# Kernel tuning notes

Measured on AMD Instinct MI355X. Metric: run time of the kernel, lower is better.

Reference implementation:

```python
import math
import jax, jax.numpy as jnp
import numpy as np
from jax import lax

RAY_START, RAY_END = 0.5, 2.5
N_PLANES = 32

# ---- camera constants (faithful to pose_spherical / fibonacci_sphere / ImagePlanes init) ----

def _pose_spherical_np(theta, phi, radius):
    trans_t = np.array([[1,0,0,0],[0,1,0,0],[0,0,1,radius],[0,0,0,1]], dtype=np.float64)
    p = phi/180.0*np.pi
    rot_phi = np.array([[1,0,0,0],[0,np.cos(p),-np.sin(p),0],[0,np.sin(p),np.cos(p),0],[0,0,0,1]], dtype=np.float64)
    t = theta/180.0*np.pi
    rot_theta = np.array([[np.cos(t),0,-np.sin(t),0],[0,1,0,0],[np.sin(t),0,np.cos(t),0],[0,0,0,1]], dtype=np.float64)
    e = 90.0/180.0*np.pi
    rot_eta = np.array([[np.cos(e),np.sin(e),0,0],[-np.sin(e),np.cos(e),0,0],[0,0,1,0],[0,0,0,1]], dtype=np.float64)
    c2w = rot_eta @ (rot_theta @ (rot_phi @ trans_t))
    return np.array([[-1,0,0,0],[0,0,1,0],[0,1,0,0],[0,0,0,1]], dtype=np.float64) @ c2w

def _fibonacci_sphere(n):
    pts = []
    golden = math.pi*(math.sqrt(5.0)-1.0)
    for i in range(n):
        y = 1 - (i/float(n-1))*2
        r = math.sqrt(1-y*y)
        th = golden*i
        x, z = math.cos(th)*r, math.sin(th)*r
        pts.append((math.atan2(z, math.sqrt(x*x+y*y)), math.atan2(y, x)))
    return pts

_poses = np.stack([_pose_spherical_np(theta, phi, -1.307) for phi, theta in _fibonacci_sphere(N_PLANES)])
_flip = np.diag(np.array([-1.0,1.0,1.0,1.0]))
POSES34 = jnp.asarray(np.stack([np.linalg.inv(p @ _flip)[:3] for p in _poses]).astype(np.float32))  # [32,3,4]
KMAT = jnp.asarray(np.array([[1.0254,0,0.5],[0,1.0254,0.5],[0,0,1]], dtype=np.float32))  # [3,3]

# ---- grid_sample(bilinear, zeros, align_corners=False) ----

def _grid_sample(img, grid):
    # img [C,H,W], grid [P,2] (x,y) in [-1,1] -> [C,P]
    C, H, W = img.shape
    ix = ((grid[:, 0] + 1.0)*W - 1.0)*0.5
    iy = ((grid[:, 1] + 1.0)*H - 1.0)*0.5
    x0 = jnp.floor(ix); y0 = jnp.floor(iy)
    wx1 = ix - x0; wy1 = iy - y0
    def tap(xx, yy, w):
        valid = (xx >= 0) & (xx <= W - 1) & (yy >= 0) & (yy <= H - 1)
        xi = jnp.clip(xx, 0, W - 1).astype(jnp.int32)
        yi = jnp.clip(yy, 0, H - 1).astype(jnp.int32)
        return img[:, yi, xi] * (w*valid)[None, :]
    return (tap(x0, y0, (1-wx1)*(1-wy1)) + tap(x0+1, y0, wx1*(1-wy1))
            + tap(x0, y0+1, (1-wx1)*wy1) + tap(x0+1, y0+1, wx1*wy1))

# ---- ImagePlanes.forward ----

def _image_plane_feats(images, points):
    # images [32,3,H,W], points [P,3] -> [P, 96+64]
    P = points.shape[0]
    ph = jnp.concatenate([points, jnp.ones((P, 1), points.dtype)], axis=1)  # [P,4]
    cam = jnp.einsum('kij,pj->kip', POSES34, ph)            # [32,3,P]
    ps = jnp.einsum('ij,kjp->kip', KMAT, cam)                # [32,3,P]
    pix = jnp.clip(ps[:, :2, :] / ps[:, 2:3, :], 0.0, 1.0)*2.0 - 1.0  # [32,2,P]
    grid = jnp.transpose(pix, (0, 2, 1))                     # [32,P,2]
    feats = jax.vmap(_grid_sample)(images, grid)             # [32,3,P]
    feats = jnp.transpose(feats, (2, 0, 1)).reshape(P, -1)   # [P,96] plane-major
    pixflat = jnp.transpose(grid, (1, 0, 2)).reshape(P, -1)  # [P,64]
    return jnp.concatenate([feats, pixflat], axis=1)

# ---- RenderNetwork.forward (only self.net path is used) ----

def _decode(x, W1, b1, W2, b2):
    h = jax.nn.softplus(x @ W1 + b1)
    o = h @ W2 + b2
    rgb = jax.nn.sigmoid(o[..., 1:])*(1.0 + 2*0.001) - 0.001
    return rgb, o[..., 0:1]

# ---- MipRayMarcher2 ----

def _ray_march(colors, densities, depths):
    deltas = depths[:, :, 1:] - depths[:, :, :-1]
    cm = (colors[:, :, :-1] + colors[:, :, 1:])*0.5
    dm = (densities[:, :, :-1] + densities[:, :, 1:])*0.5
    zm = (depths[:, :, :-1] + depths[:, :, 1:])*0.5
    dm = jax.nn.softplus(dm - 1.0)
    alpha = 1.0 - jnp.exp(-dm*deltas)
    shifted = jnp.concatenate([jnp.ones_like(alpha[:, :, :1]), 1.0 - alpha + 1e-10], axis=2)
    weights = alpha * jnp.cumprod(shifted, axis=2)[:, :, :-1]
    rgb = jnp.sum(weights*cm, axis=2)*2.0 - 1.0
    wtot = jnp.sum(weights, axis=2)
    depth = jnp.sum(weights*zm, axis=2)/wtot
    depth = jnp.clip(jnp.where(jnp.isnan(depth), jnp.inf, depth), jnp.min(depths), jnp.max(depths))
    return rgb, depth, weights

# ---- importance sampling (sample_pdf + maxpool/avgpool smoothing) ----

def _sample_pdf(bins, weights, u, eps=1e-5):
    M = weights.shape[-1]
    weights = weights + eps
    pdf = weights / jnp.sum(weights, -1, keepdims=True)
    cdf = jnp.cumsum(pdf, -1)
    cdf = jnp.concatenate([jnp.zeros_like(cdf[:, :1]), cdf], -1)  # [R,M+1]
    inds = jax.vmap(lambda c, uu: jnp.searchsorted(c, uu, side='right'))(cdf, u)
    below = jnp.maximum(inds - 1, 0)
    above = jnp.minimum(inds, M)
    cdf_b = jnp.take_along_axis(cdf, below, 1)
    cdf_a = jnp.take_along_axis(cdf, above, 1)
    bins_b = jnp.take_along_axis(bins, below, 1)
    bins_a = jnp.take_along_axis(bins, above, 1)
    denom = jnp.where(cdf_a - cdf_b < eps, 1.0, cdf_a - cdf_b)
    return bins_b + (u - cdf_b)/denom*(bins_a - bins_b)

def _sample_importance(z_vals, weights, n_imp, u):
    B, N, S, _ = z_vals.shape
    z = z_vals.reshape(B*N, S)
    w = weights.reshape(B*N, S - 1)
    wp = jnp.pad(w, ((0, 0), (1, 1)), constant_values=-jnp.inf)
    m = jnp.maximum(wp[:, :-1], wp[:, 1:])          # max_pool1d(k=2,s=1,p=1)
    sm = (m[:, :-1] + m[:, 1:])*0.5 + 0.01           # avg_pool1d(k=2,s=1)
    samples = _sample_pdf(z, sm[:, 1:-1], u.reshape(B*N, n_imp))
    return lax.stop_gradient(samples).reshape(B, N, n_imp, 1)

# ---- full ImportanceRenderer.forward ----

def _forward(planes, ray_origins, ray_directions, strat_noise, pdf_u, W1, b1, W2, b2, D, n_imp):
    B, N = ray_origins.shape[0], ray_origins.shape[1]
    H, Wd = planes.shape[-2], planes.shape[-1]
    images = planes.reshape(B, N_PLANES, 3, H, Wd)
    delta = (RAY_END - RAY_START)/(D - 1)
    depths_c = jnp.linspace(RAY_START, RAY_END, D, dtype=planes.dtype).reshape(1, 1, D, 1) + strat_noise*delta

    def run_pass(depths):
        S = depths.shape[2]
        pts = (ray_origins[:, :, None, :] + depths*ray_directions[:, :, None, :]).reshape(B, N*S, 3)
        feats = jax.vmap(_image_plane_feats)(images, pts)  # [B,N*S,160]
        rgb, sigma = _decode(feats, W1, b1, W2, b2)
        return rgb.reshape(B, N, S, 32), sigma.reshape(B, N, S, 1)

    colors_c, dens_c = run_pass(depths_c)
    _, _, w_c = _ray_march(colors_c, dens_c, depths_c)
    depths_f = _sample_importance(depths_c, w_c, n_imp, pdf_u)
    colors_f, dens_f = run_pass(depths_f)

    all_d = jnp.concatenate([depths_c, depths_f], axis=2)
    all_c = jnp.concatenate([colors_c, colors_f], axis=2)
    all_s = jnp.concatenate([dens_c, dens_f], axis=2)
    order = jnp.argsort(all_d[..., 0], axis=2)[..., None]
    all_d = jnp.take_along_axis(all_d, order, axis=2)
    all_c = jnp.take_along_axis(all_c, order, axis=2)
    all_s = jnp.take_along_axis(all_s, order, axis=2)
    rgb_final, depth_final, w = _ray_march(all_c, all_s, all_d)
    return jnp.concatenate([rgb_final, depth_final, jnp.sum(w, axis=2)], axis=-1)  # [B,N,34]


def setup_inputs() -> dict:
    key = jax.random.key(0)
    ks = jax.random.split(key, 7)
    B, N, D, NI, H = 2, 4096, 48, 48, 64
    rd = jax.random.normal(ks[2], (B, N, 3), jnp.float32)
    rd = rd / jnp.linalg.norm(rd, axis=-1, keepdims=True)
    return {
        'planes': jax.random.normal(ks[0], (B, 96, H, H), jnp.float32),
        'ray_origins': jax.random.normal(ks[1], (B, N, 3), jnp.float32)*0.1,
        'ray_directions': rd,
        'strat_noise': jax.random.uniform(ks[3], (B, N, D, 1), jnp.float32),
        'pdf_u': jax.random.uniform(ks[4], (B, N, NI), jnp.float32),
        'W1': jax.random.normal(ks[5], (160, 64), jnp.float32)*0.05,
        'b1': jnp.zeros((64,), jnp.float32),
        'W2': jax.random.normal(ks[6], (64, 33), jnp.float32)*0.05,
        'b2': jnp.zeros((33,), jnp.float32),
        'depth_resolution': 48,
        'N_importance': 48,
    }


def reference(planes, ray_origins, ray_directions, strat_noise, pdf_u, W1, b1, W2, b2, depth_resolution, N_importance):
    return _forward(planes, ray_origins, ray_directions, strat_noise, pdf_u, W1, b1, W2, b2, depth_resolution, N_importance)
```

## Files before the change

### kernel.cpp

```cpp
#include <hip/hip_runtime.h>
#include <math.h>

#define B_   2
#define N_   4096
#define S_   48
#define NPL  32
#define NRAYS (B_*N_)
#define NPTS  (NRAYS*S_)
#define DELTA_ (2.0f/47.0f)
#define NBLK_FUSED (NPTS/256)

#define ST_XS    65
#define ST_YS    66
#define ST_PLANE (ST_YS*ST_XS)
#define SETUP_GRID 66

#define OFF_POSES  0
#define OFF_MINMAX 384
#define OFF_W1E    512
#define OFF_W2E    8704
#define OFF_B2E    10240
#define OFF_ST     16384
#define OFF_DC     1114624
#define OFF_DF     1507840
#define OFF_SC     1901056
#define OFF_SF     2294272
#define OFF_CC     2687488
#define OFF_CF     8978944

typedef __attribute__((ext_vector_type(8))) short short8;
typedef __attribute__((ext_vector_type(4))) float f32x4;
typedef __attribute__((ext_vector_type(2))) float f32x2;

__device__ __forceinline__ float softplus_f(float x) {
    return fmaxf(x, 0.f) + __logf(1.f + __expf(-fabsf(x)));
}
__device__ __forceinline__ float sigmoid_f(float x) {
    return __builtin_amdgcn_rcpf(1.f + __expf(-x));
}
__device__ __forceinline__ unsigned short bf16rne(float x) {
    unsigned u = __float_as_uint(x);
    u += 0x7FFFu + ((u >> 16) & 1u);
    return (unsigned short)(u >> 16);
}
__device__ __forceinline__ unsigned bf16pk(float lo, float hi) {
    return (unsigned)bf16rne(lo) | ((unsigned)bf16rne(hi) << 16);
}
__device__ __forceinline__ float bf2f(unsigned short v) {
    return __uint_as_float(((unsigned)v) << 16);
}
__device__ __forceinline__ float bflo(unsigned u) { return __uint_as_float(u << 16); }
__device__ __forceinline__ float bfhi(unsigned u) { return __uint_as_float(u & 0xffff0000u); }
__device__ __forceinline__ f32x2 unpk2(unsigned u) { return (f32x2){bflo(u), bfhi(u)}; }
__device__ __forceinline__ int div48(int pt) {
    return (int)(((unsigned)(pt >> 4) * 43691u) >> 17);
}

__device__ void mul3(const double* a, const double* b, double* o) {
    for (int i = 0; i < 3; i++)
        for (int j = 0; j < 3; j++) {
            double s = 0.0;
            for (int k = 0; k < 3; k++) s += a[i*3+k]*b[k*3+j];
            o[i*3+j] = s;
        }
}

__global__ __launch_bounds__(256) void k_setup(
    float* ws, const float* __restrict__ W1,
    const float* __restrict__ W2, const float* __restrict__ b2,
    const float* __restrict__ planes, const float* __restrict__ noise)
{
    __shared__ unsigned short texs[3][4096];
    __shared__ float smn[4], smx[4];
    int bid = blockIdx.x;
    int t = threadIdx.x;
    if (bid == 0) {
        if (t < 32) {
            double y = 1.0 - (t/31.0)*2.0;
            double rr = sqrt(fmax(1.0 - y*y, 0.0));
            double golden = M_PI*(sqrt(5.0) - 1.0);
            double th = golden*(double)t;
            double x = cos(th)*rr, z = sin(th)*rr;
            double phi   = atan2(z, sqrt(x*x + y*y));
            double theta = atan2(y, x);
            double p  = phi/180.0*M_PI;
            double tt = theta/180.0*M_PI;
            double e  = 90.0/180.0*M_PI;
            double cp = cos(p), sp = sin(p), ct = cos(tt), st = sin(tt);
            double ce = cos(e), se = sin(e);
            double Ph[9] = {1,0,0,  0,cp,-sp,  0,sp,cp};
            double Th[9] = {ct,0,-st,  0,1,0,  st,0,ct};
            double Et[9] = {ce,se,0,  -se,ce,0,  0,0,1};
            double M3[9] = {-1,0,0,  0,0,1,  0,1,0};
            double A[9], Bm[9], R[9];
            mul3(Th, Ph, A);
            mul3(Et, A, Bm);
            mul3(M3, Bm, R);
            double radius = -1.307;
            double tv0 = radius*R[2], tv1 = radius*R[5], tv2 = radius*R[8];
            double Rf[9] = {-R[0],R[1],R[2], -R[3],R[4],R[5], -R[6],R[7],R[8]};
            float rowv[3][4];
            for (int j = 0; j < 3; j++) {
                double r0 = Rf[0*3+j], r1 = Rf[1*3+j], r2 = Rf[2*3+j];
                rowv[j][0] = (float)r0;
                rowv[j][1] = (float)r1;
                rowv[j][2] = (float)r2;
                rowv[j][3] = (float)(-(r0*tv0 + r1*tv1 + r2*tv2));
            }
            float* P = ws + OFF_POSES + t*12;
            P[0] = rowv[0][0]; P[1] = rowv[1][0];
            P[2] = rowv[0][1]; P[3] = rowv[1][1];
            P[4] = rowv[0][2]; P[5] = rowv[1][2];
            P[6] = rowv[0][3]; P[7] = rowv[1][3];
            P[8] = rowv[2][0]; P[9] = rowv[2][1]; P[10] = rowv[2][2]; P[11] = rowv[2][3];
        }
        unsigned short* w1e = (unsigned short*)(ws + OFF_W1E);
        for (int o = t; o < 64*256; o += 256) {
            int chunk = o >> 9, lane = (o >> 3) & 63, j = o & 7;
            int s = chunk >> 2, nt = chunk & 3, q = lane >> 4, n = lane & 15;
            int nn = nt*16 + n;
            int p = s*4 + q;
            float v = 0.f;
            if (j < 3)      v = W1[(3*p+j)*64 + nn];
            else if (j < 5) v = W1[(96 + 2*p + (j-3))*64 + nn];
            w1e[o] = bf16rne(v);
        }
        unsigned short* w2e = (unsigned short*)(ws + OFF_W2E);
        for (int o = t; o < 6*512; o += 256) {
            int chunk = o >> 9, lane = (o >> 3) & 63, j = o & 7;
            int nt = chunk >> 1, s2 = chunk & 1, q = lane >> 4, n = lane & 15;
            int nn = nt*16 + n;
            int k2 = s2*32 + q*8 + j;
            float v = (nn < 33) ? W2[k2*33 + nn] : 0.f;
            w2e[o] = bf16rne(v);
        }
        for (int idx = t; idx < 48; idx += 256)
            ws[OFF_B2E + idx] = (idx < 33) ? b2[idx] : 0.f;
    } else if (bid == 1) {
        float mn = 1e30f, mx = -1e30f;
        for (int r = t; r < NRAYS; r += 256) {
            float n0  = noise[(size_t)r*48];
            float n47 = noise[(size_t)r*48 + 47];
            mn = fminf(mn, 0.5f + n0*DELTA_);
            mx = fmaxf(mx, 0.5f + 47.f*DELTA_ + n47*DELTA_);
        }
        for (int off = 32; off > 0; off >>= 1) {
            mn = fminf(mn, __shfl_down(mn, off));
            mx = fmaxf(mx, __shfl_down(mx, off));
        }
        if ((t & 63) == 0) { smn[t >> 6] = mn; smx[t >> 6] = mx; }
        __syncthreads();
        if (t == 0) {
            ws[OFF_MINMAX]     = fminf(fminf(smn[0], smn[1]), fminf(smn[2], smn[3]));
            ws[OFF_MINMAX + 1] = fmaxf(fmaxf(smx[0], smx[1]), fmaxf(smx[2], smx[3]));
        }
    } else {
        int bp = bid - 2;
        int b = bp >> 5, p = bp & 31;
        const float* base = planes + ((size_t)b*96 + 3*p)*4096;
        for (int i = t; i < 4096; i += 256) {
            texs[0][i] = bf16rne(base[i]);
            texs[1][i] = bf16rne(base[4096 + i]);
            texs[2][i] = bf16rne(base[8192 + i]);
        }
        __syncthreads();
        uint4* qd = (uint4*)(ws + OFF_ST) + (size_t)bp*ST_PLANE;
        for (int e = t; e < ST_PLANE; e += 256) {
            int y = e / ST_XS, x = e - y*ST_XS;
            int jy = y - 1;
            unsigned a01 = 0, a2 = 0, b01 = 0, b2v = 0;
            if (jy >= 0 && jy <= 63) {
                int jxa = x - 1, jxb = x;
                if (jxa >= 0 && jxa <= 63) {
                    int ti = jy*64 + jxa;
                    a01 = (unsigned)texs[0][ti] | ((unsigned)texs[1][ti] << 16);
                    a2  = (unsigned)texs[2][ti];
                }
                if (jxb <= 63) {
                    int ti = jy*64 + jxb;
                    b01 = (unsigned)texs[0][ti] | ((unsigned)texs[1][ti] << 16);
                    b2v = (unsigned)texs[2][ti];
                }
            }
            qd[e] = make_uint4(a01, a2, b01, b2v);
        }
    }
}

__device__ __forceinline__ void proj_pt(
    const f32x2 Px, const f32x2 Py, const f32x2 Pz, const f32x2 Pw, const f32x4 Pc,
    float px, float py, float pz,
    int& eoff, float& wx, float& wy, unsigned& gpk)
{
    f32x2 c01 = Pz*pz + Pw;
    c01 = Py*py + c01;
    c01 = Px*px + c01;
    float c2 = fmaf(Pc.x,px, fmaf(Pc.y,py, fmaf(Pc.z,pz, Pc.w)));
    float rz = __builtin_amdgcn_rcpf(c2);
    f32x2 t01 = c01*1.0254f + 0.5f*c2;
    t01 = t01*rz;
    float cx = fminf(fmaxf(t01.x, 0.f), 1.f);
    float cy = fminf(fmaxf(t01.y, 0.f), 1.f);
    float gx = fmaf(2.f, cx, -1.f);
    float gy = fmaf(2.f, cy, -1.f);
    float ixp = fmaf(64.f, cx, 0.5f);
    float iyp = fmaf(64.f, cy, 0.5f);
    float xf = floorf(ixp), yf = floorf(iyp);
    wx = ixp - xf; wy = iyp - yf;
    eoff = (int)yf*ST_XS + (int)xf;
    gpk = bf16pk(gx, gy);
}

__device__ __forceinline__ void bilerp_pack(
    const uint4 r0, const uint4 r1, float wx, float wy, unsigned gpk, uint4& av)
{
    float wy0 = 1.f - wy, wy1 = wy;
    float w0x = 1.f - wx, w1x = wx;
    f32x2 tl01 = unpk2(r0.x)*wy0 + unpk2(r1.x)*wy1;
    float tl2  = fmaf(wy0, bflo(r0.y), wy1*bflo(r1.y));
    f32x2 tr01 = unpk2(r0.z)*wy0 + unpk2(r1.z)*wy1;
    float tr2  = fmaf(wy0, bflo(r0.w), wy1*bflo(r1.w));
    f32x2 f01 = tl01*w0x + tr01*w1x;
    float f2  = fmaf(w0x, tl2, w1x*tr2);
    av.x = bf16pk(f01.x, f01.y);
    av.y = ((unsigned)bf16rne(f2)) | (gpk << 16);
    av.z = gpk >> 16;
    av.w = 0u;
}

__global__ __launch_bounds__(512, 4) void k_fused(
    const uint4* __restrict__ stq, const float* __restrict__ poses,
    const float* __restrict__ b1, const unsigned short* __restrict__ w1e,
    const unsigned short* __restrict__ w2e, const float* __restrict__ b2e,
    unsigned short* __restrict__ colors, float* __restrict__ dens,
    const float* __restrict__ noise, const float* __restrict__ ro,
    const float* __restrict__ rd, const float* __restrict__ u,
    float* __restrict__ ws, int coarse)
{
    __shared__ __align__(16) unsigned short w1s[16384];
    __shared__ __align__(16) unsigned short w2s[3072];
    __shared__ __align__(16) unsigned short smem[8][1152];
    __shared__ __align__(16) float pl[384];
    __shared__ float impz[6][48];
    __shared__ float impcdf[6][46];
    __shared__ __align__(16) float4 posl[6][48];
    int tid = threadIdx.x;
    int wv = tid >> 6, lane = tid & 63;
    int n = lane & 15, q = lane >> 4;
    int bid = blockIdx.x;
    int swz = (bid & 7)*(NBLK_FUSED/8) + (bid >> 3);
    int wlocal = swz*256 + wv*32;
    int bq = (swz*256 >= NPTS/2) ? 32 : 0;
    int r0 = (int)(((unsigned)(swz*16) * 43691u) >> 17);

    {
        const uint4* g1 = (const uint4*)w1e;
        uint4* d1 = (uint4*)w1s;
        for (int i = tid; i < 2048; i += 512) d1[i] = g1[i];
        const uint4* g2 = (const uint4*)w2e;
        uint4* d2 = (uint4*)w2s;
        if (tid < 384) { d2[tid] = g2[tid]; pl[tid] = poses[tid]; }
    }

    if (!coarse && wv < 6) {
        int r = r0 + wv;
        const float* z   = ws + OFF_DC + (size_t)r*48;
        const float* den = ws + OFF_SC + (size_t)r*48;
        float zv = 0.f, dv = 0.f;
        if (lane < 48) { zv = z[lane]; dv = den[lane]; impz[wv][lane] = zv; }
        float zn  = __shfl_down(zv, 1);
        float dnn = __shfl_down(dv, 1);
        float alpha = 0.f, f = 1.f;
        if (lane < 47) {
            float sp = softplus_f(0.5f*(dv + dnn) - 1.f);
            alpha = 1.f - __expf(-sp*(zn - zv));
            f = 1.f - alpha + 1e-10f;
        }
        float v = f;
        for (int off = 1; off < 64; off <<= 1) { float o = __shfl_up(v, off); if (lane >= off) v *= o; }
        float T = __shfl_up(v, 1); if (lane == 0) T = 1.f;
        float w = alpha*T;
        float wn1 = __shfl_down(w, 1), wn2 = __shfl_down(w, 2);
        float pw = 0.f;
        if (lane < 45) pw = 0.5f*(fmaxf(w, wn1) + fmaxf(wn1, wn2)) + 0.01f + 1e-5f;
        float s = pw;
        for (int off = 1; off < 64; off <<= 1) { float o = __shfl_up(s, off); if (lane >= off) s += o; }
        float csum = __shfl(s, 63);
        if (lane < 45) impcdf[wv][lane+1] = s/csum;
        if (lane == 63) impcdf[wv][0] = 0.f;
        if (lane < 48) {
            float uu = u[(size_t)r*48 + lane];
            int lo = 0, hi = 46;
            while (lo < hi) { int mid = (lo+hi)>>1; if (uu >= impcdf[wv][mid]) lo = mid+1; else hi = mid; }
            int below = max(lo-1, 0), above = min(lo, 45);
            float cb = impcdf[wv][below], ca = impcdf[wv][above];
            float zb = impz[wv][below],   za = impz[wv][above];
            float dn2 = ca - cb; if (dn2 < 1e-5f) dn2 = 1.f;
            float df_s = zb + (uu - cb)/dn2*(za - zb);
            ws[OFF_DF + (size_t)r*48 + lane] = df_s;
            float fx = fmaf(df_s, rd[r*3+0], ro[r*3+0]);
            float fy = fmaf(df_s, rd[r*3+1], ro[r*3+1]);
            float fz = fmaf(df_s, rd[r*3+2], ro[r*3+2]);
            posl[wv][lane] = make_float4(fx, fy, fz, df_s);
        }
    }
    __syncthreads();

    float px[2], py[2], pz[2];
    if (coarse) {
#pragma unroll
        for (int t = 0; t < 2; t++) {
            int pt = wlocal + t*16 + n;
            int ray = div48(pt);
            int j = pt - ray*48;
            float depth = 0.5f + (float)j*DELTA_ + noise[pt]*DELTA_;
            px[t] = fmaf(depth, rd[ray*3+0], ro[ray*3+0]);
            py[t] = fmaf(depth, rd[ray*3+1], ro[ray*3+1]);
            pz[t] = fmaf(depth, rd[ray*3+2], ro[ray*3+2]);
            if (q == 0) ws[OFF_DC + pt] = depth;
        }
    } else {
#pragma unroll
        for (int t = 0; t < 2; t++) {
            int pt = wlocal + t*16 + n;
            int ray = div48(pt);
            float4 pv = posl[ray - r0][pt - ray*48];
            px[t] = pv.x; py[t] = pv.y; pz[t] = pv.z;
        }
    }

    f32x4 acc[2][4];
#pragma unroll
    for (int t = 0; t < 2; t++)
#pragma unroll
        for (int nt = 0; nt < 4; nt++) {
            float bv = b1[nt*16 + n];
            acc[t][nt] = (f32x4){bv, bv, bv, bv};
        }

#pragma unroll
    for (int s = 0; s < 8; s++) {
        int plane = s*4 + q;
        const float* Pp = pl + plane*12;
        f32x2 Px = *(const f32x2*)(Pp);
        f32x2 Py = *(const f32x2*)(Pp + 2);
        f32x2 Pz = *(const f32x2*)(Pp + 4);
        f32x2 Pw = *(const f32x2*)(Pp + 6);
        f32x4 Pc = *(const f32x4*)(Pp + 8);
        const uint4* stp = stq + (unsigned)(bq + plane)*(unsigned)ST_PLANE;
        union { short8 s8; uint4 u; } av[2];
        {
            int eo0, eo1; float wx0, wy0, wx1, wy1; unsigned g0, g1;
            proj_pt(Px, Py, Pz, Pw, Pc, px[0], py[0], pz[0], eo0, wx0, wy0, g0);
            proj_pt(Px, Py, Pz, Pw, Pc, px[1], py[1], pz[1], eo1, wx1, wy1, g1);
            uint4 a0 = stp[eo0], a1 = stp[eo0 + ST_XS];
            uint4 b0 = stp[eo1], b1r = stp[eo1 + ST_XS];
            bilerp_pack(a0, a1, wx0, wy0, g0, av[0].u);
            bilerp_pack(b0, b1r, wx1, wy1, g1, av[1].u);
        }
#pragma unroll
        for (int nt = 0; nt < 4; nt++) {
            short8 bfw = *(const short8*)(w1s + ((s*4 + nt) << 9) + (lane << 3));
#pragma unroll
            for (int t = 0; t < 2; t++)
                acc[t][nt] = __builtin_amdgcn_mfma_f32_16x16x32_bf16(av[t].s8, bfw, acc[t][nt], 0, 0, 0);
        }
    }

    short8 b2f[3][2];
#pragma unroll
    for (int nt = 0; nt < 3; nt++)
#pragma unroll
        for (int s2 = 0; s2 < 2; s2++)
            b2f[nt][s2] = *(const short8*)(w2s + (((nt << 1) | s2) << 9) + (lane << 3));

    unsigned short* ht = &smem[wv][0];
#pragma unroll
    for (int t = 0; t < 2; t++) {
#pragma unroll
        for (int nt = 0; nt < 4; nt++)
#pragma unroll
            for (int r = 0; r < 4; r++) {
                float hv = softplus_f(acc[t][nt][r]);
                ht[(q*4 + r)*72 + nt*16 + n] = bf16rne(hv);
            }
        short8 a2[2];
#pragma unroll
        for (int s2 = 0; s2 < 2; s2++)
            a2[s2] = *(const short8*)(ht + n*72 + s2*32 + q*8);

        f32x4 acc2[3];
#pragma unroll
        for (int nt = 0; nt < 3; nt++) {
            float bv = b2e[nt*16 + n];
            acc2[nt] = (f32x4){bv, bv, bv, bv};
        }
#pragma unroll
        for (int nt = 0; nt < 3; nt++)
#pragma unroll
            for (int s2 = 0; s2 < 2; s2++)
                acc2[nt] = __builtin_amdgcn_mfma_f32_16x16x32_bf16(a2[s2], b2f[nt][s2], acc2[nt], 0, 0, 0);

        float* ot = (float*)ht;
#pragma unroll
        for (int nt = 0; nt < 3; nt++) {
            int col = nt*16 + n;
#pragma unroll
            for (int r = 0; r < 4; r++) {
                float v = acc2[nt][r];
                int row = q*4 + r;
                if (col == 0) ot[row*34 + 32] = v;
                else if (col <= 32) {
                    float sg = sigmoid_f(v);
                    ot[row*34 + (col-1)] = fmaf(sg, 1.002f, -0.001f);
                }
            }
        }
        unsigned* cgu = (unsigned*)(colors + (size_t)(wlocal + t*16)*32);
#pragma unroll
        for (int i = 0; i < 4; i++) {
            int ui = i*64 + lane;
            int pt = ui >> 4, ch = (ui & 15)*2;
            cgu[ui] = bf16pk(ot[pt*34 + ch], ot[pt*34 + ch + 1]);
        }
        if (lane < 16) dens[wlocal + t*16 + lane] = ot[lane*34 + 32];
    }
}

__global__ __launch_bounds__(256) void k_final(float* __restrict__ out, const float* __restrict__ ws,
                                               const unsigned short* __restrict__ cC,
                                               const unsigned short* __restrict__ cF)
{
    __shared__ float kd[4][96];
    __shared__ float kden[4][96];
    __shared__ float sdl[4][96];
    __shared__ float sdenl[4][96];
    __shared__ int   sidxl[4][96];
    __shared__ float warr[4][96];
    __shared__ float earr[4][96];
    int tid = threadIdx.x;
    int wv = tid >> 6, lane = tid & 63;
    int r = blockIdx.x*4 + wv;
    const float* dc = ws + OFF_DC + (size_t)r*48;
    const float* df = ws + OFF_DF + (size_t)r*48;
    const float* sc = ws + OFF_SC + (size_t)r*48;
    const float* sf = ws + OFF_SF + (size_t)r*48;
    for (int i = lane; i < 96; i += 64) {
        float d, dn;
        if (i < 48) { d = dc[i]; dn = sc[i]; }
        else        { d = df[i-48]; dn = sf[i-48]; }
        kd[wv][i] = d; kden[wv][i] = dn;
    }
    __syncthreads();
    for (int i = lane; i < 96; i += 64) {
        float d = kd[wv][i];
        int rank = 0;
        for (int j = 0; j < 96; j++) {
            float dj = kd[wv][j];
            rank += (int)((dj < d) | ((dj == d) & (j < i)));
        }
        sdl[wv][rank] = d; sdenl[wv][rank] = kden[wv][i]; sidxl[wv][rank] = i;
    }
    __syncthreads();
    int i2 = 2*lane;
    float a0=0.f, f0=1.f, a1=0.f, f1=1.f, d0=0.f, d1=0.f, d2=0.f;
    if (i2 < 95) {
        d0 = sdl[wv][i2]; d1 = sdl[wv][i2+1];
        float sp = softplus_f(0.5f*(sdenl[wv][i2] + sdenl[wv][i2+1]) - 1.f);
        a0 = 1.f - __expf(-sp*(d1 - d0)); f0 = 1.f - a0 + 1e-10f;
    }
    if (i2+1 < 95) {
        d2 = sdl[wv][i2+2];
        float sp = softplus_f(0.5f*(sdenl[wv][i2+1] + sdenl[wv][i2+2]) - 1.f);
        a1 = 1.f - __expf(-sp*(d2 - d1)); f1 = 1.f - a1 + 1e-10f;
    }
    float p = f0*f1, v = p;
    for (int off = 1; off < 64; off <<= 1) { float o = __shfl_up(v, off); if (lane >= off) v *= o; }
    float excl = __shfl_up(v, 1); if (lane == 0) excl = 1.f;
    float w0 = a0*excl, w1 = a1*excl*f0;
    if (i2   < 96) warr[wv][i2]   = w0;
    if (i2+1 < 96) warr[wv][i2+1] = w1;
    float wsm = w0 + w1;
    float dsm = w0*0.5f*(d0+d1) + w1*0.5f*(d1+d2);
    for (int off = 32; off; off >>= 1) { wsm += __shfl_xor(wsm, off); dsm += __shfl_xor(dsm, off); }
    __syncthreads();
    for (int i = lane; i < 96; i += 64) {
        float wp = (i > 0)  ? warr[wv][i-1] : 0.f;
        float wc = (i < 95) ? warr[wv][i]   : 0.f;
        earr[wv][sidxl[wv][i]] = 0.5f*(wp + wc);
    }
    __syncthreads();
    int ch = lane & 31, half = lane >> 5;
    const unsigned short* cbase = (half ? cF : cC) + ((size_t)r*48)*32 + ch;
    const float* eb = &earr[wv][half*48];
    float a = 0.f;
    for (int jj = 0; jj < 48; jj++)
        a = fmaf(eb[jj], bf2f(cbase[(size_t)jj*32]), a);
    a += __shfl_xor(a, 32);
    if (lane < 32) out[(size_t)r*34 + lane] = 2.f*a - 1.f;
    if (lane == 0) {
        float gmn = ws[OFF_MINMAX];
        float gmx = ws[OFF_MINMAX + 1];
        float depth = dsm/wsm;
        if (depth != depth) depth = __builtin_inff();
        depth = fminf(fmaxf(depth, gmn), gmx);
        out[(size_t)r*34 + 32] = depth;
        out[(size_t)r*34 + 33] = wsm;
    }
}

extern "C" void kernel_launch(void* const* d_in, const int* in_sizes, int n_in,
                              void* d_out, int out_size, void* d_ws, size_t ws_size,
                              hipStream_t stream) {
    const float* planes = (const float*)d_in[0];
    const float* ro     = (const float*)d_in[1];
    const float* rd     = (const float*)d_in[2];
    const float* noise  = (const float*)d_in[3];
    const float* u      = (const float*)d_in[4];
    const float* W1     = (const float*)d_in[5];
    const float* b1     = (const float*)d_in[6];
    const float* W2     = (const float*)d_in[7];
    const float* b2     = (const float*)d_in[8];
    float* ws  = (float*)d_ws;
    float* out = (float*)d_out;
    const unsigned short* w1e = (const unsigned short*)(ws + OFF_W1E);
    const unsigned short* w2e = (const unsigned short*)(ws + OFF_W2E);
    const uint4* stq = (const uint4*)(ws + OFF_ST);
    unsigned short* cC = (unsigned short*)(ws + OFF_CC);
    unsigned short* cF = (unsigned short*)(ws + OFF_CF);

    hipLaunchKernelGGL(k_setup, dim3(SETUP_GRID), dim3(256), 0, stream,
                       ws, W1, W2, b2, planes, noise);
    hipLaunchKernelGGL(k_fused, dim3(NBLK_FUSED), dim3(512), 0, stream,
                       stq, ws + OFF_POSES, b1, w1e, w2e, ws + OFF_B2E, cC, ws + OFF_SC,
                       noise, ro, rd, u, ws, 1);
    hipLaunchKernelGGL(k_fused, dim3(NBLK_FUSED), dim3(512), 0, stream,
                       stq, ws + OFF_POSES, b1, w1e, w2e, ws + OFF_B2E, cF, ws + OFF_SF,
                       noise, ro, rd, u, ws, 0);
    hipLaunchKernelGGL(k_final, dim3(NRAYS/4), dim3(256), 0, stream, out, ws, cC, cF);
}
```

Before: 224.1 us.

## Fuse final compositing into fine pass and map one ray per wave

Each wave now handles one whole ray (48 points as three 16-row MFMA tiles) instead of 32 points that straddle rays. This lets the fine pass keep its colors and densities in LDS (reusing the weight buffer) and run the sort and composite step itself, so the separate final kernel and the fine-sample global round trip go away. The setup kernel also splits the texture-staging work into four blocks per plane. The trade-off is more registers for three accumulator tiles, and a tail of per-ray serial work inside the fused kernel that may lower occupancy.

```diff
diff --git a/kernel.cpp b/kernel.cpp
--- a/kernel.cpp
+++ b/kernel.cpp
@@ -8,12 +8,12 @@
 #define NRAYS (B_*N_)
 #define NPTS  (NRAYS*S_)
 #define DELTA_ (2.0f/47.0f)
-#define NBLK_FUSED (NPTS/256)
+#define NBLK_FUSED (NRAYS/8)
 
 #define ST_XS    65
 #define ST_YS    66
 #define ST_PLANE (ST_YS*ST_XS)
-#define SETUP_GRID 66
+#define SETUP_GRID 258
 
 #define OFF_POSES  0
 #define OFF_MINMAX 384
@@ -22,11 +22,8 @@
 #define OFF_B2E    10240
 #define OFF_ST     16384
 #define OFF_DC     1114624
-#define OFF_DF     1507840
-#define OFF_SC     1901056
-#define OFF_SF     2294272
-#define OFF_CC     2687488
-#define OFF_CF     8978944
+#define OFF_SC     1507840
+#define OFF_CC     1901056
 
 typedef __attribute__((ext_vector_type(8))) short short8;
 typedef __attribute__((ext_vector_type(4))) float f32x4;
@@ -52,9 +49,6 @@
 __device__ __forceinline__ float bflo(unsigned u) { return __uint_as_float(u << 16); }
 __device__ __forceinline__ float bfhi(unsigned u) { return __uint_as_float(u & 0xffff0000u); }
 __device__ __forceinline__ f32x2 unpk2(unsigned u) { return (f32x2){bflo(u), bfhi(u)}; }
-__device__ __forceinline__ int div48(int pt) {
-    return (int)(((unsigned)(pt >> 4) * 43691u) >> 17);
-}
 
 __device__ void mul3(const double* a, const double* b, double* o) {
     for (int i = 0; i < 3; i++)
@@ -155,7 +149,8 @@
             ws[OFF_MINMAX + 1] = fmaxf(fmaxf(smx[0], smx[1]), fmaxf(smx[2], smx[3]));
         }
     } else {
-        int bp = bid - 2;
+        int idx = bid - 2;
+        int bp = idx >> 2, part = idx & 3;
         int b = bp >> 5, p = bp & 31;
         const float* base = planes + ((size_t)b*96 + 3*p)*4096;
         for (int i = t; i < 4096; i += 256) {
@@ -165,7 +160,8 @@
         }
         __syncthreads();
         uint4* qd = (uint4*)(ws + OFF_ST) + (size_t)bp*ST_PLANE;
-        for (int e = t; e < ST_PLANE; e += 256) {
+        int e0 = part*1073, e1 = min(ST_PLANE, e0 + 1073);
+        for (int e = e0 + t; e < e1; e += 256) {
             int y = e / ST_XS, x = e - y*ST_XS;
             int jy = y - 1;
             unsigned a01 = 0, a2 = 0, b01 = 0, b2v = 0;
@@ -232,26 +228,25 @@
     const uint4* __restrict__ stq, const float* __restrict__ poses,
     const float* __restrict__ b1, const unsigned short* __restrict__ w1e,
     const unsigned short* __restrict__ w2e, const float* __restrict__ b2e,
-    unsigned short* __restrict__ colors, float* __restrict__ dens,
+    unsigned short* __restrict__ cC,
     const float* __restrict__ noise, const float* __restrict__ ro,
     const float* __restrict__ rd, const float* __restrict__ u,
-    float* __restrict__ ws, int coarse)
+    float* __restrict__ ws, float* __restrict__ out, int coarse)
 {
     __shared__ __align__(16) unsigned short w1s[16384];
     __shared__ __align__(16) unsigned short w2s[3072];
-    __shared__ __align__(16) unsigned short smem[8][1152];
+    __shared__ __align__(16) float scratch[8][672];
     __shared__ __align__(16) float pl[384];
-    __shared__ float impz[6][48];
-    __shared__ float impcdf[6][46];
-    __shared__ __align__(16) float4 posl[6][48];
+    __shared__ __align__(16) float4 posl[8][48];
+    __shared__ float densf[8][48];
     int tid = threadIdx.x;
     int wv = tid >> 6, lane = tid & 63;
     int n = lane & 15, q = lane >> 4;
     int bid = blockIdx.x;
     int swz = (bid & 7)*(NBLK_FUSED/8) + (bid >> 3);
-    int wlocal = swz*256 + wv*32;
-    int bq = (swz*256 >= NPTS/2) ? 32 : 0;
-    int r0 = (int)(((unsigned)(swz*16) * 43691u) >> 17);
+    int r = swz*8 + wv;
+    int wbase = swz*384 + wv*48;
+    int bq = (swz >= NBLK_FUSED/2) ? 32 : 0;
 
     {
         const uint4* g1 = (const uint4*)w1e;
@@ -262,12 +257,24 @@
         if (tid < 384) { d2[tid] = g2[tid]; pl[tid] = poses[tid]; }
     }
 
-    if (!coarse && wv < 6) {
-        int r = r0 + wv;
+    float px[3], py[3], pz[3];
+    if (coarse) {
+#pragma unroll
+        for (int t = 0; t < 3; t++) {
+            int j = t*16 + n;
+            float depth = 0.5f + (float)j*DELTA_ + noise[(size_t)r*48 + j]*DELTA_;
+            px[t] = fmaf(depth, rd[r*3+0], ro[r*3+0]);
+            py[t] = fmaf(depth, rd[r*3+1], ro[r*3+1]);
+            pz[t] = fmaf(depth, rd[r*3+2], ro[r*3+2]);
+            if (q == 0) ws[OFF_DC + (size_t)r*48 + j] = depth;
+        }
+    } else {
+        float* zl   = &scratch[wv][0];
+        float* cdfl = &scratch[wv][48];
         const float* z   = ws + OFF_DC + (size_t)r*48;
         const float* den = ws + OFF_SC + (size_t)r*48;
         float zv = 0.f, dv = 0.f;
-        if (lane < 48) { zv = z[lane]; dv = den[lane]; impz[wv][lane] = zv; }
+        if (lane < 48) { zv = z[lane]; dv = den[lane]; zl[lane] = zv; }
         float zn  = __shfl_down(zv, 1);
         float dnn = __shfl_down(dv, 1);
         float alpha = 0.f, f = 1.f;
@@ -286,52 +293,33 @@
         float s = pw;
         for (int off = 1; off < 64; off <<= 1) { float o = __shfl_up(s, off); if (lane >= off) s += o; }
         float csum = __shfl(s, 63);
-        if (lane < 45) impcdf[wv][lane+1] = s/csum;
-        if (lane == 63) impcdf[wv][0] = 0.f;
+        if (lane < 45) cdfl[lane+1] = s/csum;
+        if (lane == 63) cdfl[0] = 0.f;
         if (lane < 48) {
             float uu = u[(size_t)r*48 + lane];
             int lo = 0, hi = 46;
-            while (lo < hi) { int mid = (lo+hi)>>1; if (uu >= impcdf[wv][mid]) lo = mid+1; else hi = mid; }
+            while (lo < hi) { int mid = (lo+hi)>>1; if (uu >= cdfl[mid]) lo = mid+1; else hi = mid; }
             int below = max(lo-1, 0), above = min(lo, 45);
-            float cb = impcdf[wv][below], ca = impcdf[wv][above];
-            float zb = impz[wv][below],   za = impz[wv][above];
+            float cb = cdfl[below], ca = cdfl[above];
+            float zb = zl[below],   za = zl[above];
             float dn2 = ca - cb; if (dn2 < 1e-5f) dn2 = 1.f;
             float df_s = zb + (uu - cb)/dn2*(za - zb);
-            ws[OFF_DF + (size_t)r*48 + lane] = df_s;
             float fx = fmaf(df_s, rd[r*3+0], ro[r*3+0]);
             float fy = fmaf(df_s, rd[r*3+1], ro[r*3+1]);
             float fz = fmaf(df_s, rd[r*3+2], ro[r*3+2]);
             posl[wv][lane] = make_float4(fx, fy, fz, df_s);
         }
+#pragma unroll
+        for (int t = 0; t < 3; t++) {
+            float4 pv = posl[wv][t*16 + n];
+            px[t] = pv.x; py[t] = pv.y; pz[t] = pv.z;
+        }
     }
     __syncthreads();
 
-    float px[2], py[2], pz[2];
-    if (coarse) {
-#pragma unroll
-        for (int t = 0; t < 2; t++) {
-            int pt = wlocal + t*16 + n;
-            int ray = div48(pt);
-            int j = pt - ray*48;
-            float depth = 0.5f + (float)j*DELTA_ + noise[pt]*DELTA_;
-            px[t] = fmaf(depth, rd[ray*3+0], ro[ray*3+0]);
-            py[t] = fmaf(depth, rd[ray*3+1], ro[ray*3+1]);
-            pz[t] = fmaf(depth, rd[ray*3+2], ro[ray*3+2]);
-            if (q == 0) ws[OFF_DC + pt] = depth;
-        }
-    } else {
-#pragma unroll
-        for (int t = 0; t < 2; t++) {
-            int pt = wlocal + t*16 + n;
-            int ray = div48(pt);
-            float4 pv = posl[ray - r0][pt - ray*48];
-            px[t] = pv.x; py[t] = pv.y; pz[t] = pv.z;
-        }
-    }
-
-    f32x4 acc[2][4];
-#pragma unroll
-    for (int t = 0; t < 2; t++)
+    f32x4 acc[3][4];
+#pragma unroll
+    for (int t = 0; t < 3; t++)
 #pragma unroll
         for (int nt = 0; nt < 4; nt++) {
             float bv = b1[nt*16 + n];
@@ -348,21 +336,24 @@
         f32x2 Pw = *(const f32x2*)(Pp + 6);
         f32x4 Pc = *(const f32x4*)(Pp + 8);
         const uint4* stp = stq + (unsigned)(bq + plane)*(unsigned)ST_PLANE;
-        union { short8 s8; uint4 u; } av[2];
+        union { short8 s8; uint4 u; } av[3];
         {
-            int eo0, eo1; float wx0, wy0, wx1, wy1; unsigned g0, g1;
+            int eo0, eo1, eo2; float wx0, wy0, wx1, wy1, wx2, wy2; unsigned g0, g1, g2;
             proj_pt(Px, Py, Pz, Pw, Pc, px[0], py[0], pz[0], eo0, wx0, wy0, g0);
             proj_pt(Px, Py, Pz, Pw, Pc, px[1], py[1], pz[1], eo1, wx1, wy1, g1);
+            proj_pt(Px, Py, Pz, Pw, Pc, px[2], py[2], pz[2], eo2, wx2, wy2, g2);
             uint4 a0 = stp[eo0], a1 = stp[eo0 + ST_XS];
             uint4 b0 = stp[eo1], b1r = stp[eo1 + ST_XS];
+            uint4 c0 = stp[eo2], c1r = stp[eo2 + ST_XS];
             bilerp_pack(a0, a1, wx0, wy0, g0, av[0].u);
             bilerp_pack(b0, b1r, wx1, wy1, g1, av[1].u);
+            bilerp_pack(c0, c1r, wx2, wy2, g2, av[2].u);
         }
 #pragma unroll
         for (int nt = 0; nt < 4; nt++) {
             short8 bfw = *(const short8*)(w1s + ((s*4 + nt) << 9) + (lane << 3));
 #pragma unroll
-            for (int t = 0; t < 2; t++)
+            for (int t = 0; t < 3; t++)
                 acc[t][nt] = __builtin_amdgcn_mfma_f32_16x16x32_bf16(av[t].s8, bfw, acc[t][nt], 0, 0, 0);
         }
     }
@@ -374,15 +365,17 @@
         for (int s2 = 0; s2 < 2; s2++)
             b2f[nt][s2] = *(const short8*)(w2s + (((nt << 1) | s2) << 9) + (lane << 3));
 
-    unsigned short* ht = &smem[wv][0];
-#pragma unroll
-    for (int t = 0; t < 2; t++) {
+    __syncthreads();
+
+    unsigned short* ht = (unsigned short*)&scratch[wv][0];
+#pragma unroll
+    for (int t = 0; t < 3; t++) {
 #pragma unroll
         for (int nt = 0; nt < 4; nt++)
 #pragma unroll
-            for (int r = 0; r < 4; r++) {
-                float hv = softplus_f(acc[t][nt][r]);
-                ht[(q*4 + r)*72 + nt*16 + n] = bf16rne(hv);
+            for (int r2 = 0; r2 < 4; r2++) {
+                float hv = softplus_f(acc[t][nt][r2]);
+                ht[(q*4 + r2)*72 + nt*16 + n] = bf16rne(hv);
             }
         short8 a2[2];
 #pragma unroll
@@ -406,9 +399,9 @@
         for (int nt = 0; nt < 3; nt++) {
             int col = nt*16 + n;
 #pragma unroll
-            for (int r = 0; r < 4; r++) {
-                float v = acc2[nt][r];
-                int row = q*4 + r;
+            for (int r2 = 0; r2 < 4; r2++) {
+                float v = acc2[nt][r2];
+                int row = q*4 + r2;
                 if (col == 0) ot[row*34 + 32] = v;
                 else if (col <= 32) {
                     float sg = sigmoid_f(v);
@@ -416,86 +409,90 @@
                 }
             }
         }
-        unsigned* cgu = (unsigned*)(colors + (size_t)(wlocal + t*16)*32);
-#pragma unroll
-        for (int i = 0; i < 4; i++) {
-            int ui = i*64 + lane;
-            int pt = ui >> 4, ch = (ui & 15)*2;
-            cgu[ui] = bf16pk(ot[pt*34 + ch], ot[pt*34 + ch + 1]);
-        }
-        if (lane < 16) dens[wlocal + t*16 + lane] = ot[lane*34 + 32];
-    }
-}
-
-__global__ __launch_bounds__(256) void k_final(float* __restrict__ out, const float* __restrict__ ws,
-                                               const unsigned short* __restrict__ cC,
-                                               const unsigned short* __restrict__ cF)
-{
-    __shared__ float kd[4][96];
-    __shared__ float kden[4][96];
-    __shared__ float sdl[4][96];
-    __shared__ float sdenl[4][96];
-    __shared__ int   sidxl[4][96];
-    __shared__ float warr[4][96];
-    __shared__ float earr[4][96];
-    int tid = threadIdx.x;
-    int wv = tid >> 6, lane = tid & 63;
-    int r = blockIdx.x*4 + wv;
+        if (coarse) {
+            unsigned* cgu = (unsigned*)(cC + (size_t)(wbase + t*16)*32);
+#pragma unroll
+            for (int i = 0; i < 4; i++) {
+                int ui = i*64 + lane;
+                int pt = ui >> 4, ch = (ui & 15)*2;
+                cgu[ui] = bf16pk(ot[pt*34 + ch], ot[pt*34 + ch + 1]);
+            }
+            if (lane < 16) ws[OFF_SC + (size_t)(wbase + t*16 + lane)] = ot[lane*34 + 32];
+        } else {
+            unsigned* cgl = (unsigned*)w1s + (size_t)(wv*48 + t*16)*16;
+#pragma unroll
+            for (int i = 0; i < 4; i++) {
+                int ui = i*64 + lane;
+                int pt = ui >> 4, ch = (ui & 15)*2;
+                cgl[ui] = bf16pk(ot[pt*34 + ch], ot[pt*34 + ch + 1]);
+            }
+            if (lane < 16) densf[wv][t*16 + lane] = ot[lane*34 + 32];
+        }
+    }
+
+    if (coarse) return;
+
+    float* kd    = &scratch[wv][0];
+    float* kden  = kd + 96;
+    float* sdl   = kd + 192;
+    float* sdenl = kd + 288;
+    int*   sidx  = (int*)(kd + 384);
+    float* warr  = kd + 480;
+    float* earr  = kd + 576;
     const float* dc = ws + OFF_DC + (size_t)r*48;
-    const float* df = ws + OFF_DF + (size_t)r*48;
     const float* sc = ws + OFF_SC + (size_t)r*48;
-    const float* sf = ws + OFF_SF + (size_t)r*48;
     for (int i = lane; i < 96; i += 64) {
         float d, dn;
         if (i < 48) { d = dc[i]; dn = sc[i]; }
-        else        { d = df[i-48]; dn = sf[i-48]; }
-        kd[wv][i] = d; kden[wv][i] = dn;
-    }
-    __syncthreads();
+        else        { d = posl[wv][i-48].w; dn = densf[wv][i-48]; }
+        kd[i] = d; kden[i] = dn;
+    }
     for (int i = lane; i < 96; i += 64) {
-        float d = kd[wv][i];
+        float d = kd[i];
         int rank = 0;
         for (int j = 0; j < 96; j++) {
-            float dj = kd[wv][j];
+            float dj = kd[j];
             rank += (int)((dj < d) | ((dj == d) & (j < i)));
         }
-        sdl[wv][rank] = d; sdenl[wv][rank] = kden[wv][i]; sidxl[wv][rank] = i;
-    }
-    __syncthreads();
+        sdl[rank] = d; sdenl[rank] = kden[i]; sidx[rank] = i;
+    }
     int i2 = 2*lane;
     float a0=0.f, f0=1.f, a1=0.f, f1=1.f, d0=0.f, d1=0.f, d2=0.f;
     if (i2 < 95) {
-        d0 = sdl[wv][i2]; d1 = sdl[wv][i2+1];
-        float sp = softplus_f(0.5f*(sdenl[wv][i2] + sdenl[wv][i2+1]) - 1.f);
+        d0 = sdl[i2]; d1 = sdl[i2+1];
+        float sp = softplus_f(0.5f*(sdenl[i2] + sdenl[i2+1]) - 1.f);
         a0 = 1.f - __expf(-sp*(d1 - d0)); f0 = 1.f - a0 + 1e-10f;
     }
     if (i2+1 < 95) {
-        d2 = sdl[wv][i2+2];
-        float sp = softplus_f(0.5f*(sdenl[wv][i2+1] + sdenl[wv][i2+2]) - 1.f);
+        d2 = sdl[i2+2];
+        float sp = softplus_f(0.5f*(sdenl[i2+1] + sdenl[i2+2]) - 1.f);
         a1 = 1.f - __expf(-sp*(d2 - d1)); f1 = 1.f - a1 + 1e-10f;
     }
     float p = f0*f1, v = p;
     for (int off = 1; off < 64; off <<= 1) { float o = __shfl_up(v, off); if (lane >= off) v *= o; }
     float excl = __shfl_up(v, 1); if (lane == 0) excl = 1.f;
     float w0 = a0*excl, w1 = a1*excl*f0;
-    if (i2   < 96) warr[wv][i2]   = w0;
-    if (i2+1 < 96) warr[wv][i2+1] = w1;
+    if (i2   < 96) warr[i2]   = w0;
+    if (i2+1 < 96) warr[i2+1] = w1;
     float wsm = w0 + w1;
     float dsm = w0*0.5f*(d0+d1) + w1*0.5f*(d1+d2);
     for (int off = 32; off; off >>= 1) { wsm += __shfl_xor(wsm, off); dsm += __shfl_xor(dsm, off); }
-    __syncthreads();
     for (int i = lane; i < 96; i += 64) {
-        float wp = (i > 0)  ? warr[wv][i-1] : 0.f;
-        float wc = (i < 95) ? warr[wv][i]   : 0.f;
-        earr[wv][sidxl[wv][i]] = 0.5f*(wp + wc);
-    }
-    __syncthreads();
+        float wp = (i > 0)  ? warr[i-1] : 0.f;
+        float wc = (i < 95) ? warr[i]   : 0.f;
+        earr[sidx[i]] = 0.5f*(wp + wc);
+    }
     int ch = lane & 31, half = lane >> 5;
-    const unsigned short* cbase = (half ? cF : cC) + ((size_t)r*48)*32 + ch;
-    const float* eb = &earr[wv][half*48];
     float a = 0.f;
-    for (int jj = 0; jj < 48; jj++)
-        a = fmaf(eb[jj], bf2f(cbase[(size_t)jj*32]), a);
+    if (half == 0) {
+        const unsigned short* cbase = cC + (size_t)r*48*32 + ch;
+        for (int jj = 0; jj < 48; jj++)
+            a = fmaf(earr[jj], bf2f(cbase[(size_t)jj*32]), a);
+    } else {
+        const unsigned short* cbase = w1s + (size_t)(wv*48)*32 + ch;
+        for (int jj = 0; jj < 48; jj++)
+            a = fmaf(earr[48 + jj], bf2f(cbase[(size_t)jj*32]), a);
+    }
     a += __shfl_xor(a, 32);
     if (lane < 32) out[(size_t)r*34 + lane] = 2.f*a - 1.f;
     if (lane == 0) {
@@ -527,15 +524,13 @@
     const unsigned short* w2e = (const unsigned short*)(ws + OFF_W2E);
     const uint4* stq = (const uint4*)(ws + OFF_ST);
     unsigned short* cC = (unsigned short*)(ws + OFF_CC);
-    unsigned short* cF = (unsigned short*)(ws + OFF_CF);
 
     hipLaunchKernelGGL(k_setup, dim3(SETUP_GRID), dim3(256), 0, stream,
                        ws, W1, W2, b2, planes, noise);
     hipLaunchKernelGGL(k_fused, dim3(NBLK_FUSED), dim3(512), 0, stream,
-                       stq, ws + OFF_POSES, b1, w1e, w2e, ws + OFF_B2E, cC, ws + OFF_SC,
-                       noise, ro, rd, u, ws, 1);
+                       stq, ws + OFF_POSES, b1, w1e, w2e, ws + OFF_B2E, cC,
+                       noise, ro, rd, u, ws, out, 1);
     hipLaunchKernelGGL(k_fused, dim3(NBLK_FUSED), dim3(512), 0, stream,
-                       stq, ws + OFF_POSES, b1, w1e, w2e, ws + OFF_B2E, cF, ws + OFF_SF,
-                       noise, ro, rd, u, ws, 0);
-    hipLaunchKernelGGL(k_final, dim3(NRAYS/4), dim3(256), 0, stream, out, ws, cC, cF);
-}
+                       stq, ws + OFF_POSES, b1, w1e, w2e, ws + OFF_B2E, cC,
+                       noise, ro, rd, u, ws, out, 0);
+}
```

Result: no change. 228.1 us (+1.8%).
